# Kernel tuning notes

Hardware: AMD Instinct MI355X
Metric: run time of the kernel (lower is better)

## Reference

```python
import jax, jax.numpy as jnp
import numpy as np

INPUT_DIM = 1024
EMBED_DIMS = 128


def setup_inputs() -> dict:
    key = jax.random.key(0)
    ks = jax.random.split(key, 7)
    s_in = 1.0 / np.sqrt(INPUT_DIM)
    x = jax.random.normal(ks[0], (4, 4096, INPUT_DIM), dtype=jnp.float32)
    Wq = jax.random.uniform(ks[1], (INPUT_DIM, EMBED_DIMS), jnp.float32, -s_in, s_in)
    bq = jax.random.uniform(ks[2], (EMBED_DIMS,), jnp.float32, -s_in, s_in)
    Wk = jax.random.uniform(ks[3], (INPUT_DIM, EMBED_DIMS), jnp.float32, -s_in, s_in)
    bk = jax.random.uniform(ks[4], (EMBED_DIMS,), jnp.float32, -s_in, s_in)
    Wv = jax.random.uniform(ks[5], (INPUT_DIM, EMBED_DIMS), jnp.float32, -s_in, s_in)
    bv = jax.random.uniform(ks[6], (EMBED_DIMS,), jnp.float32, -s_in, s_in)
    return {"x": x, "Wq": Wq, "bq": bq, "Wk": Wk, "bk": bk, "Wv": Wv, "bv": bv}


def reference(x, Wq, bq, Wk, bk, Wv, bv):
    # x: [B, L, C]
    Q = jnp.einsum('blc,cd->bld', x, Wq) + bq  # [B, L, D]
    K = jnp.einsum('blc,cd->bld', x, Wk) + bk
    V = jnp.einsum('blc,cd->bld', x, Wv) + bv
    d_k = Q.shape[-1]
    scores = jnp.einsum('bld,bmd->blm', Q, K) / jnp.sqrt(jnp.float32(d_k))  # [B, L, L]
    attn = jax.nn.softmax(scores, axis=-1)
    return jnp.einsum('blm,bmd->bld', attn, V)  # [B, L, D]
```

## Files before the change

### kernel.cpp

```cpp
#include <hip/hip_runtime.h>
#include <stdint.h>

typedef __bf16 bf16;
typedef __bf16 bf16x8 __attribute__((ext_vector_type(8)));
typedef __bf16 bf16x4 __attribute__((ext_vector_type(4)));
typedef float f32x4 __attribute__((ext_vector_type(4)));

#define LQ    16384
#define CDIM  1024
#define DDIM  128
#define NSPLIT 4
#define SCALE 0.08838834764831845f

__global__ void wtrans_kernel(const float* __restrict__ Wq, const float* __restrict__ Wk,
                              const float* __restrict__ Wv, bf16* __restrict__ Wt3) {
  int idx = blockIdx.x * 256 + threadIdx.x;
  int y = idx >> 17;
  int rem = idx & 131071;
  int k = rem >> 7, n = rem & 127;
  const float* W = (y == 0) ? Wq : (y == 1) ? Wk : Wv;
  Wt3[(size_t)y * 131072 + (size_t)n * CDIM + k] = (bf16)W[rem];
}

__global__ __launch_bounds__(256, 3) void qkv_gemm(
    const float* __restrict__ x, const bf16* __restrict__ Wt3,
    const float* __restrict__ bq, const float* __restrict__ bk, const float* __restrict__ bv,
    bf16* __restrict__ Qw, bf16* __restrict__ Kw, bf16* __restrict__ Vtw) {
  __shared__ bf16 Al[64 * 72];
  __shared__ bf16 Bl[128 * 72];
  const int t = threadIdx.x;
  const int w = t >> 6;
  const int lane = t & 63;
  const int l15 = lane & 15;
  const int quad = lane >> 4;
  const int y = blockIdx.y;
  const int m0 = blockIdx.x * 64;
  const bf16* W = Wt3 + (size_t)y * (DDIM * CDIM);
  const float* bias = (y == 0) ? bq : (y == 1) ? bk : bv;
  const int m_off = (w & 1) * 32;
  const int n_off = (w >> 1) * 64;
  const int xr = t >> 4;
  const int xc = (t & 15) << 2;
  const int wr = t >> 3;
  const int wc = (t & 7) << 3;

  f32x4 zero4 = {0.f, 0.f, 0.f, 0.f};
  f32x4 acc[2][4];
#pragma unroll
  for (int i = 0; i < 2; i++)
#pragma unroll
    for (int j = 0; j < 4; j++) acc[i][j] = zero4;

  float4 xa[4];
  bf16x8 wa[4];
#pragma unroll
  for (int c = 0; c < 4; c++)
    xa[c] = *(const float4*)&x[(size_t)(m0 + c * 16 + xr) * CDIM + xc];
#pragma unroll
  for (int c = 0; c < 4; c++)
    wa[c] = *(const bf16x8*)&W[(size_t)(c * 32 + wr) * CDIM + wc];

  for (int kc = 0; kc < 16; kc++) {
    __syncthreads();
#pragma unroll
    for (int c = 0; c < 4; c++) {
      bf16x4 v;
      v[0] = (bf16)xa[c].x; v[1] = (bf16)xa[c].y;
      v[2] = (bf16)xa[c].z; v[3] = (bf16)xa[c].w;
      *(bf16x4*)&Al[(c * 16 + xr) * 72 + xc] = v;
    }
#pragma unroll
    for (int c = 0; c < 4; c++)
      *(bf16x8*)&Bl[(c * 32 + wr) * 72 + wc] = wa[c];
    __syncthreads();

    const int kn = (kc < 15 ? kc + 1 : 15) * 64;
#pragma unroll
    for (int c = 0; c < 4; c++)
      xa[c] = *(const float4*)&x[(size_t)(m0 + c * 16 + xr) * CDIM + kn + xc];
#pragma unroll
    for (int c = 0; c < 4; c++)
      wa[c] = *(const bf16x8*)&W[(size_t)(c * 32 + wr) * CDIM + kn + wc];

#pragma unroll
    for (int ks = 0; ks < 2; ks++) {
      bf16x8 af[2], bfr[4];
#pragma unroll
      for (int mt = 0; mt < 2; mt++)
        af[mt] = *(const bf16x8*)&Al[(m_off + mt * 16 + l15) * 72 + ks * 32 + quad * 8];
#pragma unroll
      for (int nt = 0; nt < 4; nt++)
        bfr[nt] = *(const bf16x8*)&Bl[(n_off + nt * 16 + l15) * 72 + ks * 32 + quad * 8];
#pragma unroll
      for (int mt = 0; mt < 2; mt++)
#pragma unroll
        for (int nt = 0; nt < 4; nt++)
          acc[mt][nt] = __builtin_amdgcn_mfma_f32_16x16x32_bf16(af[mt], bfr[nt], acc[mt][nt], 0, 0, 0);
    }
  }

  float bias4[4];
#pragma unroll
  for (int nt = 0; nt < 4; nt++) bias4[nt] = bias[n_off + nt * 16 + l15];

  if (y < 2) {
    bf16* out = (y == 0) ? Qw : Kw;
#pragma unroll
    for (int mt = 0; mt < 2; mt++)
#pragma unroll
      for (int nt = 0; nt < 4; nt++) {
        int n = n_off + nt * 16 + l15;
#pragma unroll
        for (int r = 0; r < 4; r++) {
          int m = m0 + m_off + mt * 16 + quad * 4 + r;
          out[(size_t)m * DDIM + n] = (bf16)(acc[mt][nt][r] + bias4[nt]);
        }
      }
  } else {
#pragma unroll
    for (int mt = 0; mt < 2; mt++)
#pragma unroll
      for (int nt = 0; nt < 4; nt++) {
        int n = n_off + nt * 16 + l15;
        int m = m0 + m_off + mt * 16 + quad * 4;
        bf16x4 pv;
#pragma unroll
        for (int r = 0; r < 4; r++) pv[r] = (bf16)(acc[mt][nt][r] + bias4[nt]);
        *(bf16x4*)&Vtw[(size_t)n * LQ + m] = pv;
      }
  }
}

__global__ __launch_bounds__(256, 2) void flash_kernel(
    const bf16* __restrict__ Qw, const bf16* __restrict__ Kw, const bf16* __restrict__ Vtw,
    bf16* __restrict__ Opb, float2* __restrict__ ml) {
  __shared__ bf16 Kl[64 * 136];
  __shared__ bf16 Vl[128 * 72];
  __shared__ bf16 Pl[4 * 32 * 72];

  const int t = threadIdx.x;
  const int w = t >> 6;
  const int lane = t & 63;
  const int l15 = lane & 15;
  const int quad = lane >> 4;
  const int qb = blockIdx.x;
  const int sp = blockIdx.y;
  const int batch = qb >> 5;
  const int q0w = qb * 128 + w * 32;
  const int kv_base = batch * 4096 + sp * 1024;

  bf16x8 qf[2][4];
#pragma unroll
  for (int mt = 0; mt < 2; mt++)
#pragma unroll
    for (int ks = 0; ks < 4; ks++)
      qf[mt][ks] = *(const bf16x8*)&Qw[(size_t)(q0w + mt * 16 + l15) * DDIM + ks * 32 + quad * 8];

  f32x4 zero4 = {0.f, 0.f, 0.f, 0.f};
  f32x4 o[2][8];
#pragma unroll
  for (int mt = 0; mt < 2; mt++)
#pragma unroll
    for (int dt = 0; dt < 8; dt++) o[mt][dt] = zero4;
  float mi[2][4], li[2][4];
#pragma unroll
  for (int mt = 0; mt < 2; mt++)
#pragma unroll
    for (int r = 0; r < 4; r++) { mi[mt][r] = -INFINITY; li[mt][r] = 0.f; }

  bf16* Pw = Pl + w * (32 * 72);
  const int kr = t >> 4;
  const int kcol = (t & 15) << 3;
  const int vr = t >> 3;
  const int vcol = (t & 7) << 3;

  bf16x8 ka[4], va[4];
#pragma unroll
  for (int c = 0; c < 4; c++)
    ka[c] = *(const bf16x8*)&Kw[(size_t)(kv_base + c * 16 + kr) * DDIM + kcol];
#pragma unroll
  for (int c = 0; c < 4; c++)
    va[c] = *(const bf16x8*)&Vtw[(size_t)(c * 32 + vr) * LQ + kv_base + vcol];

  for (int tile = 0; tile < 16; tile++) {
    __syncthreads();
#pragma unroll
    for (int c = 0; c < 4; c++)
      *(bf16x8*)&Kl[(c * 16 + kr) * 136 + kcol] = ka[c];
#pragma unroll
    for (int c = 0; c < 4; c++)
      *(bf16x8*)&Vl[(c * 32 + vr) * 72 + vcol] = va[c];
    __syncthreads();

    const int kvn = kv_base + (tile < 15 ? tile + 1 : 15) * 64;
#pragma unroll
    for (int c = 0; c < 4; c++)
      ka[c] = *(const bf16x8*)&Kw[(size_t)(kvn + c * 16 + kr) * DDIM + kcol];
#pragma unroll
    for (int c = 0; c < 4; c++)
      va[c] = *(const bf16x8*)&Vtw[(size_t)(c * 32 + vr) * LQ + kvn + vcol];

    f32x4 sv[2][4];
#pragma unroll
    for (int mt = 0; mt < 2; mt++)
#pragma unroll
      for (int nt = 0; nt < 4; nt++) sv[mt][nt] = zero4;
#pragma unroll
    for (int ks = 0; ks < 4; ks++) {
      bf16x8 kf[4];
#pragma unroll
      for (int nt = 0; nt < 4; nt++)
        kf[nt] = *(const bf16x8*)&Kl[(nt * 16 + l15) * 136 + ks * 32 + quad * 8];
#pragma unroll
      for (int mt = 0; mt < 2; mt++)
#pragma unroll
        for (int nt = 0; nt < 4; nt++)
          sv[mt][nt] = __builtin_amdgcn_mfma_f32_16x16x32_bf16(qf[mt][ks], kf[nt], sv[mt][nt], 0, 0, 0);
    }
#pragma unroll
    for (int mt = 0; mt < 2; mt++)
#pragma unroll
      for (int nt = 0; nt < 4; nt++) sv[mt][nt] *= SCALE;

#pragma unroll
    for (int mt = 0; mt < 2; mt++) {
#pragma unroll
      for (int r = 0; r < 4; r++) {
        float rm = fmaxf(fmaxf(sv[mt][0][r], sv[mt][1][r]), fmaxf(sv[mt][2][r], sv[mt][3][r]));
#pragma unroll
        for (int msk = 1; msk < 16; msk <<= 1) rm = fmaxf(rm, __shfl_xor(rm, msk));
        float mnew = fmaxf(mi[mt][r], rm);
        float alpha = __expf(mi[mt][r] - mnew);
        mi[mt][r] = mnew;
        float rsum = 0.f;
#pragma unroll
        for (int nt = 0; nt < 4; nt++) {
          float p = __expf(sv[mt][nt][r] - mnew);
          sv[mt][nt][r] = p;
          rsum += p;
        }
#pragma unroll
        for (int msk = 1; msk < 16; msk <<= 1) rsum += __shfl_xor(rsum, msk);
        li[mt][r] = li[mt][r] * alpha + rsum;
#pragma unroll
        for (int dt = 0; dt < 8; dt++) o[mt][dt][r] *= alpha;
      }
    }

#pragma unroll
    for (int mt = 0; mt < 2; mt++)
#pragma unroll
      for (int nt = 0; nt < 4; nt++)
#pragma unroll
        for (int r = 0; r < 4; r++)
          Pw[(mt * 16 + quad * 4 + r) * 72 + nt * 16 + l15] = (bf16)sv[mt][nt][r];

#pragma unroll
    for (int ks = 0; ks < 2; ks++) {
      bf16x8 pf[2];
#pragma unroll
      for (int mt = 0; mt < 2; mt++)
        pf[mt] = *(const bf16x8*)&Pw[(mt * 16 + l15) * 72 + ks * 32 + quad * 8];
#pragma unroll
      for (int dt = 0; dt < 8; dt++) {
        bf16x8 vf = *(const bf16x8*)&Vl[(dt * 16 + l15) * 72 + ks * 32 + quad * 8];
#pragma unroll
        for (int mt = 0; mt < 2; mt++)
          o[mt][dt] = __builtin_amdgcn_mfma_f32_16x16x32_bf16(pf[mt], vf, o[mt][dt], 0, 0, 0);
      }
    }
  }

  const size_t po = (size_t)sp * LQ * DDIM;
#pragma unroll
  for (int mt = 0; mt < 2; mt++)
#pragma unroll
    for (int dt = 0; dt < 8; dt++)
#pragma unroll
      for (int r = 0; r < 4; r++)
        Opb[po + (size_t)(q0w + mt * 16 + quad * 4 + r) * DDIM + dt * 16 + l15] = (bf16)o[mt][dt][r];
  if (l15 == 0) {
#pragma unroll
    for (int mt = 0; mt < 2; mt++)
#pragma unroll
      for (int r = 0; r < 4; r++)
        ml[(size_t)sp * LQ + q0w + mt * 16 + quad * 4 + r] = make_float2(mi[mt][r], li[mt][r]);
  }
}

__global__ void combine_kernel(const bf16* __restrict__ Opb, const float2* __restrict__ ml,
                               float* __restrict__ out) {
  int idx = blockIdx.x * 256 + threadIdx.x;
  int q = idx >> 5;
  int d = (idx & 31) * 4;
  float m[NSPLIT], l[NSPLIT];
  float M = -INFINITY;
#pragma unroll
  for (int sp = 0; sp < NSPLIT; sp++) {
    float2 a = ml[(size_t)sp * LQ + q];
    m[sp] = a.x; l[sp] = a.y;
    M = fmaxf(M, a.x);
  }
  float wsum = 0.f;
  float acc[4] = {0.f, 0.f, 0.f, 0.f};
#pragma unroll
  for (int sp = 0; sp < NSPLIT; sp++) {
    float wgt = __expf(m[sp] - M);
    wsum += wgt * l[sp];
    bf16x4 ov = *(const bf16x4*)&Opb[(size_t)sp * LQ * DDIM + (size_t)q * DDIM + d];
#pragma unroll
    for (int j = 0; j < 4; j++) acc[j] += wgt * (float)ov[j];
  }
  float inv = 1.0f / wsum;
  float4 r;
  r.x = acc[0] * inv; r.y = acc[1] * inv; r.z = acc[2] * inv; r.w = acc[3] * inv;
  *(float4*)&out[(size_t)q * DDIM + d] = r;
}

extern "C" void kernel_launch(void* const* d_in, const int* in_sizes, int n_in,
                              void* d_out, int out_size, void* d_ws, size_t ws_size,
                              hipStream_t stream) {
  const float* x  = (const float*)d_in[0];
  const float* Wq = (const float*)d_in[1];
  const float* bq = (const float*)d_in[2];
  const float* Wk = (const float*)d_in[3];
  const float* bk = (const float*)d_in[4];
  const float* Wv = (const float*)d_in[5];
  const float* bv = (const float*)d_in[6];
  char* ws = (char*)d_ws;
  bf16* Qw  = (bf16*)(ws);
  bf16* Kw  = (bf16*)(ws + ((size_t)4 << 20));
  bf16* Vtw = (bf16*)(ws + ((size_t)8 << 20));
  bf16* Wt3 = (bf16*)(ws + ((size_t)12 << 20));
  bf16* Opb = (bf16*)(ws + ((size_t)12 << 20) + 786432);
  float2* mlp = (float2*)(ws + ((size_t)12 << 20) + 786432 + ((size_t)16 << 20));
  float* out = (float*)d_out;

  wtrans_kernel<<<1536, 256, 0, stream>>>(Wq, Wk, Wv, Wt3);
  qkv_gemm<<<dim3(256, 3), 256, 0, stream>>>(x, Wt3, bq, bk, bv, Qw, Kw, Vtw);
  flash_kernel<<<dim3(128, NSPLIT), 256, 0, stream>>>(Qw, Kw, Vtw, Opb, mlp);
  combine_kernel<<<2048, 256, 0, stream>>>(Opb, mlp, out);
}
```

Measured before the change: 200.1 us.

## Fuse QKV projections per block, fold softmax scale into Wq, MFMA row sums

```diff
diff --git a/kernel.cpp b/kernel.cpp
--- a/kernel.cpp
+++ b/kernel.cpp
@@ -10,133 +10,130 @@
 #define CDIM  1024
 #define DDIM  128
 #define NSPLIT 4
-#define SCALE 0.08838834764831845f
-
-__global__ void wtrans_kernel(const float* __restrict__ Wq, const float* __restrict__ Wk,
-                              const float* __restrict__ Wv, bf16* __restrict__ Wt3) {
+#define QS 0.12751741f
+
+__device__ __forceinline__ float dppmax_xor1(float v) {
+  float t = __uint_as_float(__builtin_amdgcn_mov_dpp(__float_as_uint(v), 0xB1, 0xF, 0xF, true));
+  return fmaxf(v, t);
+}
+__device__ __forceinline__ float dppmax_xor2(float v) {
+  float t = __uint_as_float(__builtin_amdgcn_mov_dpp(__float_as_uint(v), 0x4E, 0xF, 0xF, true));
+  return fmaxf(v, t);
+}
+
+__global__ void prep_kernel(const float* __restrict__ Wq, const float* __restrict__ Wk,
+                            const float* __restrict__ Wv, const float* __restrict__ bq,
+                            const float* __restrict__ bk, const float* __restrict__ bv,
+                            bf16* __restrict__ Wt, float* __restrict__ bias_all) {
   int idx = blockIdx.x * 256 + threadIdx.x;
-  int y = idx >> 17;
+  int p = idx >> 17;
   int rem = idx & 131071;
   int k = rem >> 7, n = rem & 127;
-  const float* W = (y == 0) ? Wq : (y == 1) ? Wk : Wv;
-  Wt3[(size_t)y * 131072 + (size_t)n * CDIM + k] = (bf16)W[rem];
-}
-
-__global__ __launch_bounds__(256, 3) void qkv_gemm(
-    const float* __restrict__ x, const bf16* __restrict__ Wt3,
-    const float* __restrict__ bq, const float* __restrict__ bk, const float* __restrict__ bv,
+  const float* W = (p == 0) ? Wq : (p == 1) ? Wk : Wv;
+  float s = (p == 0) ? QS : 1.0f;
+  Wt[(size_t)(p * 128 + n) * CDIM + k] = (bf16)(W[rem] * s);
+  if (idx < 384) {
+    int pp = idx >> 7, nn = idx & 127;
+    const float* b = (pp == 0) ? bq : (pp == 1) ? bk : bv;
+    bias_all[idx] = b[nn] * ((pp == 0) ? QS : 1.0f);
+  }
+}
+
+__global__ __launch_bounds__(256, 2) void qkv_gemm(
+    const float* __restrict__ x, const bf16* __restrict__ Wt,
+    const float* __restrict__ bias_all,
     bf16* __restrict__ Qw, bf16* __restrict__ Kw, bf16* __restrict__ Vtw) {
-  __shared__ bf16 Al[64 * 72];
-  __shared__ bf16 Bl[128 * 72];
+  __shared__ bf16 Al[32 * 72];
+  __shared__ bf16 Bl[384 * 72];
   const int t = threadIdx.x;
   const int w = t >> 6;
   const int lane = t & 63;
   const int l15 = lane & 15;
   const int quad = lane >> 4;
-  const int y = blockIdx.y;
-  const int m0 = blockIdx.x * 64;
-  const bf16* W = Wt3 + (size_t)y * (DDIM * CDIM);
-  const float* bias = (y == 0) ? bq : (y == 1) ? bk : bv;
-  const int m_off = (w & 1) * 32;
-  const int n_off = (w >> 1) * 64;
-  const int xr = t >> 4;
-  const int xc = (t & 15) << 2;
-  const int wr = t >> 3;
-  const int wc = (t & 7) << 3;
+  const int m0 = blockIdx.x * 32;
+  const int n_off = w * 96;
+  const int ar = t >> 3, ac = (t & 7) << 3;
+  const int br = t >> 3, bc = (t & 7) << 3;
 
   f32x4 zero4 = {0.f, 0.f, 0.f, 0.f};
-  f32x4 acc[2][4];
+  f32x4 acc[2][6];
 #pragma unroll
   for (int i = 0; i < 2; i++)
 #pragma unroll
-    for (int j = 0; j < 4; j++) acc[i][j] = zero4;
-
-  float4 xa[4];
-  bf16x8 wa[4];
-#pragma unroll
-  for (int c = 0; c < 4; c++)
-    xa[c] = *(const float4*)&x[(size_t)(m0 + c * 16 + xr) * CDIM + xc];
-#pragma unroll
-  for (int c = 0; c < 4; c++)
-    wa[c] = *(const bf16x8*)&W[(size_t)(c * 32 + wr) * CDIM + wc];
+    for (int j = 0; j < 6; j++) acc[i][j] = zero4;
+
+  float4 xa[2];
+  bf16x8 wb[12];
+  xa[0] = *(const float4*)&x[(size_t)(m0 + ar) * CDIM + ac];
+  xa[1] = *(const float4*)&x[(size_t)(m0 + ar) * CDIM + ac + 4];
+#pragma unroll
+  for (int c = 0; c < 12; c++)
+    wb[c] = *(const bf16x8*)&Wt[(size_t)(c * 32 + br) * CDIM + bc];
 
   for (int kc = 0; kc < 16; kc++) {
     __syncthreads();
-#pragma unroll
-    for (int c = 0; c < 4; c++) {
-      bf16x4 v;
-      v[0] = (bf16)xa[c].x; v[1] = (bf16)xa[c].y;
-      v[2] = (bf16)xa[c].z; v[3] = (bf16)xa[c].w;
-      *(bf16x4*)&Al[(c * 16 + xr) * 72 + xc] = v;
-    }
-#pragma unroll
-    for (int c = 0; c < 4; c++)
-      *(bf16x8*)&Bl[(c * 32 + wr) * 72 + wc] = wa[c];
+    {
+      bf16x8 av;
+      av[0] = (bf16)xa[0].x; av[1] = (bf16)xa[0].y; av[2] = (bf16)xa[0].z; av[3] = (bf16)xa[0].w;
+      av[4] = (bf16)xa[1].x; av[5] = (bf16)xa[1].y; av[6] = (bf16)xa[1].z; av[7] = (bf16)xa[1].w;
+      *(bf16x8*)&Al[ar * 72 + ac] = av;
+    }
+#pragma unroll
+    for (int c = 0; c < 12; c++)
+      *(bf16x8*)&Bl[(c * 32 + br) * 72 + bc] = wb[c];
     __syncthreads();
 
     const int kn = (kc < 15 ? kc + 1 : 15) * 64;
-#pragma unroll
-    for (int c = 0; c < 4; c++)
-      xa[c] = *(const float4*)&x[(size_t)(m0 + c * 16 + xr) * CDIM + kn + xc];
-#pragma unroll
-    for (int c = 0; c < 4; c++)
-      wa[c] = *(const bf16x8*)&W[(size_t)(c * 32 + wr) * CDIM + kn + wc];
+    xa[0] = *(const float4*)&x[(size_t)(m0 + ar) * CDIM + kn + ac];
+    xa[1] = *(const float4*)&x[(size_t)(m0 + ar) * CDIM + kn + ac + 4];
+#pragma unroll
+    for (int c = 0; c < 12; c++)
+      wb[c] = *(const bf16x8*)&Wt[(size_t)(c * 32 + br) * CDIM + kn + bc];
 
 #pragma unroll
     for (int ks = 0; ks < 2; ks++) {
-      bf16x8 af[2], bfr[4];
+      bf16x8 af[2], bfr[6];
 #pragma unroll
       for (int mt = 0; mt < 2; mt++)
-        af[mt] = *(const bf16x8*)&Al[(m_off + mt * 16 + l15) * 72 + ks * 32 + quad * 8];
-#pragma unroll
-      for (int nt = 0; nt < 4; nt++)
+        af[mt] = *(const bf16x8*)&Al[(mt * 16 + l15) * 72 + ks * 32 + quad * 8];
+#pragma unroll
+      for (int nt = 0; nt < 6; nt++)
         bfr[nt] = *(const bf16x8*)&Bl[(n_off + nt * 16 + l15) * 72 + ks * 32 + quad * 8];
 #pragma unroll
       for (int mt = 0; mt < 2; mt++)
 #pragma unroll
-        for (int nt = 0; nt < 4; nt++)
+        for (int nt = 0; nt < 6; nt++)
           acc[mt][nt] = __builtin_amdgcn_mfma_f32_16x16x32_bf16(af[mt], bfr[nt], acc[mt][nt], 0, 0, 0);
     }
   }
 
-  float bias4[4];
-#pragma unroll
-  for (int nt = 0; nt < 4; nt++) bias4[nt] = bias[n_off + nt * 16 + l15];
-
-  if (y < 2) {
-    bf16* out = (y == 0) ? Qw : Kw;
-#pragma unroll
-    for (int mt = 0; mt < 2; mt++)
-#pragma unroll
-      for (int nt = 0; nt < 4; nt++) {
-        int n = n_off + nt * 16 + l15;
-#pragma unroll
-        for (int r = 0; r < 4; r++) {
-          int m = m0 + m_off + mt * 16 + quad * 4 + r;
-          out[(size_t)m * DDIM + n] = (bf16)(acc[mt][nt][r] + bias4[nt]);
-        }
+#pragma unroll
+  for (int mt = 0; mt < 2; mt++)
+#pragma unroll
+    for (int nt = 0; nt < 6; nt++) {
+      int n = n_off + nt * 16 + l15;
+      int proj = n >> 7, nl = n & 127;
+      float b = bias_all[n];
+      int m = m0 + mt * 16 + quad * 4;
+      if (proj == 2) {
+        bf16x4 pv;
+#pragma unroll
+        for (int r = 0; r < 4; r++) pv[r] = (bf16)(acc[mt][nt][r] + b);
+        *(bf16x4*)&Vtw[(size_t)nl * LQ + m] = pv;
+      } else {
+        bf16* outp = (proj == 0) ? Qw : Kw;
+#pragma unroll
+        for (int r = 0; r < 4; r++)
+          outp[(size_t)(m + r) * DDIM + nl] = (bf16)(acc[mt][nt][r] + b);
       }
-  } else {
-#pragma unroll
-    for (int mt = 0; mt < 2; mt++)
-#pragma unroll
-      for (int nt = 0; nt < 4; nt++) {
-        int n = n_off + nt * 16 + l15;
-        int m = m0 + m_off + mt * 16 + quad * 4;
-        bf16x4 pv;
-#pragma unroll
-        for (int r = 0; r < 4; r++) pv[r] = (bf16)(acc[mt][nt][r] + bias4[nt]);
-        *(bf16x4*)&Vtw[(size_t)n * LQ + m] = pv;
-      }
-  }
-}
-
-__global__ __launch_bounds__(256, 2) void flash_kernel(
+    }
+}
+
+__global__ __launch_bounds__(128, 2) void flash_kernel(
     const bf16* __restrict__ Qw, const bf16* __restrict__ Kw, const bf16* __restrict__ Vtw,
     bf16* __restrict__ Opb, float2* __restrict__ ml) {
-  __shared__ bf16 Kl[64 * 136];
+  __shared__ bf16 KP[64 * 136];
   __shared__ bf16 Vl[128 * 72];
-  __shared__ bf16 Pl[4 * 32 * 72];
 
   const int t = threadIdx.x;
   const int w = t >> 6;
@@ -145,8 +142,8 @@
   const int quad = lane >> 4;
   const int qb = blockIdx.x;
   const int sp = blockIdx.y;
-  const int batch = qb >> 5;
-  const int q0w = qb * 128 + w * 32;
+  const int batch = qb >> 6;
+  const int q0w = qb * 64 + w * 32;
   const int kv_base = batch * 4096 + sp * 1024;
 
   bf16x8 qf[2][4];
@@ -168,37 +165,41 @@
 #pragma unroll
     for (int r = 0; r < 4; r++) { mi[mt][r] = -INFINITY; li[mt][r] = 0.f; }
 
-  bf16* Pw = Pl + w * (32 * 72);
+  bf16* Pw = KP + w * (32 * 68);
   const int kr = t >> 4;
   const int kcol = (t & 15) << 3;
   const int vr = t >> 3;
   const int vcol = (t & 7) << 3;
 
-  bf16x8 ka[4], va[4];
-#pragma unroll
-  for (int c = 0; c < 4; c++)
-    ka[c] = *(const bf16x8*)&Kw[(size_t)(kv_base + c * 16 + kr) * DDIM + kcol];
-#pragma unroll
-  for (int c = 0; c < 4; c++)
-    va[c] = *(const bf16x8*)&Vtw[(size_t)(c * 32 + vr) * LQ + kv_base + vcol];
+  bf16x8 onef;
+#pragma unroll
+  for (int i = 0; i < 8; i++) onef[i] = (bf16)1.0f;
+
+  bf16x8 ka[8], va[8];
+#pragma unroll
+  for (int c = 0; c < 8; c++)
+    ka[c] = *(const bf16x8*)&Kw[(size_t)(kv_base + c * 8 + kr) * DDIM + kcol];
+#pragma unroll
+  for (int c = 0; c < 8; c++)
+    va[c] = *(const bf16x8*)&Vtw[(size_t)(c * 16 + vr) * LQ + kv_base + vcol];
 
   for (int tile = 0; tile < 16; tile++) {
     __syncthreads();
 #pragma unroll
-    for (int c = 0; c < 4; c++)
-      *(bf16x8*)&Kl[(c * 16 + kr) * 136 + kcol] = ka[c];
-#pragma unroll
-    for (int c = 0; c < 4; c++)
-      *(bf16x8*)&Vl[(c * 32 + vr) * 72 + vcol] = va[c];
+    for (int c = 0; c < 8; c++)
+      *(bf16x8*)&KP[(c * 8 + kr) * 136 + kcol] = ka[c];
+#pragma unroll
+    for (int c = 0; c < 8; c++)
+      *(bf16x8*)&Vl[(c * 16 + vr) * 72 + vcol] = va[c];
     __syncthreads();
 
     const int kvn = kv_base + (tile < 15 ? tile + 1 : 15) * 64;
 #pragma unroll
-    for (int c = 0; c < 4; c++)
-      ka[c] = *(const bf16x8*)&Kw[(size_t)(kvn + c * 16 + kr) * DDIM + kcol];
-#pragma unroll
-    for (int c = 0; c < 4; c++)
-      va[c] = *(const bf16x8*)&Vtw[(size_t)(c * 32 + vr) * LQ + kvn + vcol];
+    for (int c = 0; c < 8; c++)
+      ka[c] = *(const bf16x8*)&Kw[(size_t)(kvn + c * 8 + kr) * DDIM + kcol];
+#pragma unroll
+    for (int c = 0; c < 8; c++)
+      va[c] = *(const bf16x8*)&Vtw[(size_t)(c * 16 + vr) * LQ + kvn + vcol];
 
     f32x4 sv[2][4];
 #pragma unroll
@@ -210,57 +211,59 @@
       bf16x8 kf[4];
 #pragma unroll
       for (int nt = 0; nt < 4; nt++)
-        kf[nt] = *(const bf16x8*)&Kl[(nt * 16 + l15) * 136 + ks * 32 + quad * 8];
+        kf[nt] = *(const bf16x8*)&KP[(nt * 16 + l15) * 136 + ks * 32 + quad * 8];
 #pragma unroll
       for (int mt = 0; mt < 2; mt++)
 #pragma unroll
         for (int nt = 0; nt < 4; nt++)
           sv[mt][nt] = __builtin_amdgcn_mfma_f32_16x16x32_bf16(qf[mt][ks], kf[nt], sv[mt][nt], 0, 0, 0);
     }
-#pragma unroll
-    for (int mt = 0; mt < 2; mt++)
-#pragma unroll
-      for (int nt = 0; nt < 4; nt++) sv[mt][nt] *= SCALE;
-
+
+    float alf[2][4];
 #pragma unroll
     for (int mt = 0; mt < 2; mt++) {
 #pragma unroll
       for (int r = 0; r < 4; r++) {
         float rm = fmaxf(fmaxf(sv[mt][0][r], sv[mt][1][r]), fmaxf(sv[mt][2][r], sv[mt][3][r]));
-#pragma unroll
-        for (int msk = 1; msk < 16; msk <<= 1) rm = fmaxf(rm, __shfl_xor(rm, msk));
+        rm = dppmax_xor1(rm);
+        rm = dppmax_xor2(rm);
+        rm = fmaxf(rm, __shfl_xor(rm, 4));
+        rm = fmaxf(rm, __shfl_xor(rm, 8));
         float mnew = fmaxf(mi[mt][r], rm);
-        float alpha = __expf(mi[mt][r] - mnew);
+        float alpha = exp2f(mi[mt][r] - mnew);
         mi[mt][r] = mnew;
-        float rsum = 0.f;
-#pragma unroll
-        for (int nt = 0; nt < 4; nt++) {
-          float p = __expf(sv[mt][nt][r] - mnew);
-          sv[mt][nt][r] = p;
-          rsum += p;
-        }
-#pragma unroll
-        for (int msk = 1; msk < 16; msk <<= 1) rsum += __shfl_xor(rsum, msk);
-        li[mt][r] = li[mt][r] * alpha + rsum;
+        alf[mt][r] = alpha;
+#pragma unroll
+        for (int nt = 0; nt < 4; nt++)
+          sv[mt][nt][r] = exp2f(sv[mt][nt][r] - mnew);
 #pragma unroll
         for (int dt = 0; dt < 8; dt++) o[mt][dt][r] *= alpha;
       }
     }
 
+    __syncthreads();
 #pragma unroll
     for (int mt = 0; mt < 2; mt++)
 #pragma unroll
       for (int nt = 0; nt < 4; nt++)
 #pragma unroll
         for (int r = 0; r < 4; r++)
-          Pw[(mt * 16 + quad * 4 + r) * 72 + nt * 16 + l15] = (bf16)sv[mt][nt][r];
-
+          Pw[(mt * 16 + quad * 4 + r) * 68 + nt * 16 + l15] = (bf16)sv[mt][nt][r];
+
+    f32x4 rs[2];
+    rs[0] = zero4; rs[1] = zero4;
 #pragma unroll
     for (int ks = 0; ks < 2; ks++) {
       bf16x8 pf[2];
 #pragma unroll
+      for (int mt = 0; mt < 2; mt++) {
+        bf16x4 plo = *(const bf16x4*)&Pw[(mt * 16 + l15) * 68 + ks * 32 + quad * 8];
+        bf16x4 phi = *(const bf16x4*)&Pw[(mt * 16 + l15) * 68 + ks * 32 + quad * 8 + 4];
+        pf[mt] = __builtin_shufflevector(plo, phi, 0, 1, 2, 3, 4, 5, 6, 7);
+      }
+#pragma unroll
       for (int mt = 0; mt < 2; mt++)
-        pf[mt] = *(const bf16x8*)&Pw[(mt * 16 + l15) * 72 + ks * 32 + quad * 8];
+        rs[mt] = __builtin_amdgcn_mfma_f32_16x16x32_bf16(pf[mt], onef, rs[mt], 0, 0, 0);
 #pragma unroll
       for (int dt = 0; dt < 8; dt++) {
         bf16x8 vf = *(const bf16x8*)&Vl[(dt * 16 + l15) * 72 + ks * 32 + quad * 8];
@@ -269,6 +272,11 @@
           o[mt][dt] = __builtin_amdgcn_mfma_f32_16x16x32_bf16(pf[mt], vf, o[mt][dt], 0, 0, 0);
       }
     }
+#pragma unroll
+    for (int mt = 0; mt < 2; mt++)
+#pragma unroll
+      for (int r = 0; r < 4; r++)
+        li[mt][r] = li[mt][r] * alf[mt][r] + rs[mt][r];
   }
 
   const size_t po = (size_t)sp * LQ * DDIM;
@@ -305,7 +313,7 @@
   float acc[4] = {0.f, 0.f, 0.f, 0.f};
 #pragma unroll
   for (int sp = 0; sp < NSPLIT; sp++) {
-    float wgt = __expf(m[sp] - M);
+    float wgt = exp2f(m[sp] - M);
     wsum += wgt * l[sp];
     bf16x4 ov = *(const bf16x4*)&Opb[(size_t)sp * LQ * DDIM + (size_t)q * DDIM + d];
 #pragma unroll
@@ -328,16 +336,17 @@
   const float* Wv = (const float*)d_in[5];
   const float* bv = (const float*)d_in[6];
   char* ws = (char*)d_ws;
-  bf16* Qw  = (bf16*)(ws);
-  bf16* Kw  = (bf16*)(ws + ((size_t)4 << 20));
-  bf16* Vtw = (bf16*)(ws + ((size_t)8 << 20));
-  bf16* Wt3 = (bf16*)(ws + ((size_t)12 << 20));
-  bf16* Opb = (bf16*)(ws + ((size_t)12 << 20) + 786432);
-  float2* mlp = (float2*)(ws + ((size_t)12 << 20) + 786432 + ((size_t)16 << 20));
+  bf16* Qw   = (bf16*)(ws);
+  bf16* Kw   = (bf16*)(ws + ((size_t)4 << 20));
+  bf16* Vtw  = (bf16*)(ws + ((size_t)8 << 20));
+  bf16* Wt   = (bf16*)(ws + ((size_t)12 << 20));
+  float* bias_all = (float*)(ws + ((size_t)12 << 20) + 786432);
+  bf16* Opb  = (bf16*)(ws + ((size_t)13 << 20));
+  float2* mlp = (float2*)(ws + ((size_t)29 << 20));
   float* out = (float*)d_out;
 
-  wtrans_kernel<<<1536, 256, 0, stream>>>(Wq, Wk, Wv, Wt3);
-  qkv_gemm<<<dim3(256, 3), 256, 0, stream>>>(x, Wt3, bq, bk, bv, Qw, Kw, Vtw);
-  flash_kernel<<<dim3(128, NSPLIT), 256, 0, stream>>>(Qw, Kw, Vtw, Opb, mlp);
+  prep_kernel<<<1536, 256, 0, stream>>>(Wq, Wk, Wv, bq, bk, bv, Wt, bias_all);
+  qkv_gemm<<<512, 256, 0, stream>>>(x, Wt, bias_all, Qw, Kw, Vtw);
+  flash_kernel<<<dim3(256, NSPLIT), 128, 0, stream>>>(Qw, Kw, Vtw, Opb, mlp);
   combine_kernel<<<2048, 256, 0, stream>>>(Opb, mlp, out);
 }
```

After: 210.1 us. 5.0% more time.
